# Kernel optimization log

Hardware: AMD Instinct MI355X
Metric: run time of the kernel (lower is better)

Reference implementation:

```python
import jax, jax.numpy as jnp
import numpy as np
from jax import lax

BN_EPS = 1e-5

def ste_sign(x):
    # forward: sign(x) (sign(0)=0, matching torch.sign); backward handled in fwdbwd variant
    return jnp.sign(x)

def setup_inputs() -> dict:
    key = jax.random.key(0)
    k1, k2, k3 = jax.random.split(key, 3)
    x = jax.random.normal(k1, (32, 256, 56, 56), dtype=jnp.float32)
    gamma = jnp.ones((256,), dtype=jnp.float32)
    beta = jnp.zeros((256,), dtype=jnp.float32)
    weight = jax.random.normal(k2, (256, 256, 3, 3), dtype=jnp.float32) * 0.05
    bias = jax.random.normal(k3, (256,), dtype=jnp.float32) * 0.05
    return {"x": x, "gamma": gamma, "beta": beta, "weight": weight, "bias": bias}

def reference(x, gamma, beta, weight, bias):
    # shuffle_groups == 1 -> no channel shuffle
    # BatchNorm2d in training mode: batch statistics over (N, H, W)
    mean = jnp.mean(x, axis=(0, 2, 3), keepdims=True)          # (1,C,1,1)
    var = jnp.var(x, axis=(0, 2, 3), keepdims=True)
    xn = (x - mean) * lax.rsqrt(var + BN_EPS)
    xn = xn * gamma[None, :, None, None] + beta[None, :, None, None]
    # Binary activation: sign
    xb = ste_sign(xn)
    # Binarized-weight conv (weights -> sign(W)), stride 1, padding 1
    wb = ste_sign(weight)
    y = lax.conv_general_dilated(
        xb, wb,
        window_strides=(1, 1),
        padding=[(1, 1), (1, 1)],
        dimension_numbers=("NCHW", "OIHW", "NCHW"),
    )
    y = y + bias[None, :, None, None]
    return jax.nn.relu(y)
```

## Files before the change

### kernel.cpp

```cpp
#include <hip/hip_runtime.h>
#include <stdint.h>


#define CH   256
#define HH   56
#define WW   56
#define HWSZ (HH*WW)
#define NBATCH 32
#define NHW  (NBATCH*HWSZ)


__global__ __launch_bounds__(256) void bn_stats(const float* __restrict__ x,
                                                float* __restrict__ stats,
                                                unsigned* __restrict__ flags) {
    int c = blockIdx.x;
    const float4* xp = (const float4*)x;
    double s = 0.0, s2 = 0.0;
    for (int idx = threadIdx.x; idx < NBATCH * 784; idx += 256) {
        int n = idx / 784, i = idx - n * 784;
        float4 v = xp[(size_t)(n * CH + c) * 784 + i];
        s  += (double)v.x + (double)v.y + (double)v.z + (double)v.w;
        s2 += (double)v.x * v.x + (double)v.y * v.y
            + (double)v.z * v.z + (double)v.w * v.w;
    }
    __shared__ double ls[256], ls2[256];
    ls[threadIdx.x] = s; ls2[threadIdx.x] = s2;
    __syncthreads();
    for (int o = 128; o > 0; o >>= 1) {
        if (threadIdx.x < o) {
            ls[threadIdx.x]  += ls[threadIdx.x + o];
            ls2[threadIdx.x] += ls2[threadIdx.x + o];
        }
        __syncthreads();
    }
    if (threadIdx.x == 0) {
        double mean = ls[0] / (double)NHW;
        double var  = ls2[0] / (double)NHW - mean * mean;
        double istd = 1.0 / sqrt(var + 1e-5);
        stats[2 * c]     = (float)mean;
        stats[2 * c + 1] = (float)istd;
        if (c == 0) *flags = 0u;
    }
}

__global__ __launch_bounds__(256) void binarize(const float* __restrict__ x,
                                                const float* __restrict__ gamma,
                                                const float* __restrict__ beta,
                                                const float* __restrict__ stats,
                                                unsigned long long* __restrict__ Apack,
                                                unsigned long long* __restrict__ Amask,
                                                unsigned* __restrict__ flags) {
    int b = blockIdx.x;
    int n = b / HH, h = b - n * HH;
    __shared__ float lds[CH][WW + 1];
    for (int i = threadIdx.x; i < CH * WW; i += 256) {
        int ci = i / WW, w = i - ci * WW;
        lds[ci][w] = x[(size_t)(n * CH + ci) * HWSZ + h * WW + w];
    }
    __syncthreads();
    int ci = threadIdx.x;
    float m = stats[2 * ci], istd = stats[2 * ci + 1];
    float g = gamma[ci], bb = beta[ci];
    int wv = threadIdx.x >> 6, lane = threadIdx.x & 63;
    bool anyz = false;
    size_t pixbase = (size_t)(n * HH + h) * WW * 4;
    for (int w = 0; w < WW; ++w) {
        float xn = (lds[ci][w] - m) * istd;
        xn = xn * g + bb;
        unsigned long long sb = __ballot(xn > 0.0f);
        unsigned long long mb = __ballot(xn != 0.0f);
        anyz |= (xn == 0.0f);
        if (lane == 0) {
            Apack[pixbase + w * 4 + wv] = sb;
            Amask[pixbase + w * 4 + wv] = mb;
        }
    }
    if (__any(anyz)) { if (lane == 0) atomicOr(flags, 1u); }
}

__global__ __launch_bounds__(128) void packw(const float* __restrict__ wt,
                                             unsigned* __restrict__ Wsign,
                                             unsigned* __restrict__ Wmask,
                                             unsigned* __restrict__ flags) {
    int co = blockIdx.x, t = threadIdx.x;
    if (t >= 72) return;
    int tap = t >> 3, word = t & 7;
    unsigned sb = 0u, mb = 0u;
    for (int j = 0; j < 32; ++j) {
        float v = wt[((size_t)co * CH + (word * 32 + j)) * 9 + tap];
        sb |= (v > 0.0f ? 1u : 0u) << j;
        mb |= (v != 0.0f ? 1u : 0u) << j;
    }
    Wsign[(co * 9 + tap) * 8 + word] = sb;
    Wmask[(co * 9 + tap) * 8 + word] = mb;
    if (mb != 0xffffffffu) atomicOr(flags, 2u);
}

__global__ __launch_bounds__(256) void bconv(const uint32_t* __restrict__ Apack,
                                             const uint32_t* __restrict__ Amask,
                                             const uint32_t* __restrict__ Wsign,
                                             const uint32_t* __restrict__ Wmask,
                                             const float* __restrict__ bias,
                                             const unsigned* __restrict__ flags,
                                             float* __restrict__ out) {
    int b = blockIdx.x;
    int n = b / 28, tb = b - n * 28;
    int h0 = tb * 2;
    int co = threadIdx.x;

    __shared__ __align__(16) uint32_t As[4][WW][8];
    __shared__ __align__(16) uint32_t Am[4][WW][8];

    bool slow = (*flags != 0u);

    int rlo = max(h0 - 1, 0), rhi = min(h0 + 2, HH - 1);
    int nw = (rhi - rlo + 1) * WW * 8;
    {
        const uint4* s4 = (const uint4*)(Apack + (size_t)(n * HH + rlo) * WW * 8);
        uint4* d4 = (uint4*)&As[rlo - (h0 - 1)][0][0];
        for (int i = threadIdx.x; i < nw / 4; i += 256) d4[i] = s4[i];
        if (slow) {
            const uint4* s4m = (const uint4*)(Amask + (size_t)(n * HH + rlo) * WW * 8);
            uint4* d4m = (uint4*)&Am[rlo - (h0 - 1)][0][0];
            for (int i = threadIdx.x; i < nw / 4; i += 256) d4m[i] = s4m[i];
        }
    }

    uint32_t wreg[72];
    #pragma unroll
    for (int i = 0; i < 72; ++i) wreg[i] = Wsign[co * 72 + i];
    float bi = bias[co];
    __syncthreads();

    if (!slow) {
        for (int r = 0; r < 2; ++r) {
            int h = h0 + r;
            size_t obase = (size_t)(n * CH + co) * HWSZ + (size_t)h * WW;
            for (int c = 0; c < WW; ++c) {
                int acc = 0, kcnt = 0;
                #pragma unroll
                for (int kh = 0; kh < 3; ++kh) {
                    int hh = h - 1 + kh;
                    if (hh < 0 || hh >= HH) continue;
                    int lr = r + kh;
                    #pragma unroll
                    for (int kw = 0; kw < 3; ++kw) {
                        int wwc = c - 1 + kw;
                        if (wwc < 0 || wwc >= WW) continue;
                        const uint32_t* ap = &As[lr][wwc][0];
                        #pragma unroll
                        for (int k = 0; k < 8; ++k)
                            acc += __popc(ap[k] ^ wreg[(kh * 3 + kw) * 8 + k]);
                        kcnt += 256;
                    }
                }
                float o = (float)(kcnt - 2 * acc) + bi;
                out[obase + c] = o > 0.0f ? o : 0.0f;
            }
        }
    } else {
        for (int r = 0; r < 2; ++r) {
            int h = h0 + r;
            size_t obase = (size_t)(n * CH + co) * HWSZ + (size_t)h * WW;
            for (int c = 0; c < WW; ++c) {
                int acc = 0, kcnt = 0;
                #pragma unroll
                for (int kh = 0; kh < 3; ++kh) {
                    int hh = h - 1 + kh;
                    if (hh < 0 || hh >= HH) continue;
                    int lr = r + kh;
                    #pragma unroll
                    for (int kw = 0; kw < 3; ++kw) {
                        int wwc = c - 1 + kw;
                        if (wwc < 0 || wwc >= WW) continue;
                        const uint32_t* ap = &As[lr][wwc][0];
                        const uint32_t* am = &Am[lr][wwc][0];
                        const uint32_t* wm = Wmask + (co * 9 + kh * 3 + kw) * 8;
                        #pragma unroll
                        for (int k = 0; k < 8; ++k) {
                            uint32_t M = am[k] & wm[k];
                            kcnt += __popc(M);
                            acc  += __popc((ap[k] ^ wreg[(kh * 3 + kw) * 8 + k]) & M);
                        }
                    }
                }
                float o = (float)(kcnt - 2 * acc) + bi;
                out[obase + c] = o > 0.0f ? o : 0.0f;
            }
        }
    }
}

extern "C" void kernel_launch(void* const* d_in, const int* in_sizes, int n_in,
                              void* d_out, int out_size, void* d_ws, size_t ws_size,
                              hipStream_t stream) {
    const float* x     = (const float*)d_in[0];
    const float* gamma = (const float*)d_in[1];
    const float* beta  = (const float*)d_in[2];
    const float* wt    = (const float*)d_in[3];
    const float* bias  = (const float*)d_in[4];
    float* out = (float*)d_out;

    char* ws = (char*)d_ws;
    float*    stats = (float*)(ws);
    unsigned* flags = (unsigned*)(ws + 2048);
    uint32_t* Wsign = (uint32_t*)(ws + 4096);
    uint32_t* Wmask = (uint32_t*)(ws + 77824);
    uint32_t* Apack = (uint32_t*)(ws + 151552);
    uint32_t* Amask = (uint32_t*)(ws + 3362816);

    hipLaunchKernelGGL(bn_stats, dim3(256), dim3(256), 0, stream, x, stats, flags);
    hipLaunchKernelGGL(binarize, dim3(NBATCH * HH), dim3(256), 0, stream,
                       x, gamma, beta, stats,
                       (unsigned long long*)Apack, (unsigned long long*)Amask, flags);
    hipLaunchKernelGGL(packw, dim3(256), dim3(128), 0, stream, wt, Wsign, Wmask, flags);
    hipLaunchKernelGGL(bconv, dim3(NBATCH * 28), dim3(256), 0, stream,
                       Apack, Amask, Wsign, Wmask, bias, flags, out);
}
```

Measured before the change: 481.2 us.

## Split BN stats, stage binarize writes, and restructure fast binary conv per-pixel

Batch-norm statistics now run as a two-stage reduction over (channel, batch) blocks with wave shuffles, which spreads the work across many more workgroups. Binarize loads with float4 and writes its packed words through LDS as coalesced uint4 stores. The fast convolution path is rewritten so each thread holds one pixel's zero-padded 3x3 window in registers and loops over output channels, reading broadcast weights. A precomputed per-border correction term replaces the per-tap boundary branches. The slow masked path moves to a separate kernel that exits early when not needed, which adds an extra launch, and the 72-word register window may limit occupancy.

```diff
diff --git a/kernel.cpp b/kernel.cpp
--- a/kernel.cpp
+++ b/kernel.cpp
@@ -10,37 +10,46 @@
 #define NHW  (NBATCH*HWSZ)
 
 
-__global__ __launch_bounds__(256) void bn_stats(const float* __restrict__ x,
-                                                float* __restrict__ stats,
-                                                unsigned* __restrict__ flags) {
-    int c = blockIdx.x;
-    const float4* xp = (const float4*)x;
+__global__ __launch_bounds__(256) void bn_partial(const float* __restrict__ x,
+                                                  double* __restrict__ psum,
+                                                  double* __restrict__ psum2) {
+    int b = blockIdx.x;
+    int c = b >> 5, n = b & 31;
+    const float4* x4 = (const float4*)x + (size_t)(n * CH + c) * 784;
     double s = 0.0, s2 = 0.0;
-    for (int idx = threadIdx.x; idx < NBATCH * 784; idx += 256) {
-        int n = idx / 784, i = idx - n * 784;
-        float4 v = xp[(size_t)(n * CH + c) * 784 + i];
+    for (int i = threadIdx.x; i < 784; i += 256) {
+        float4 v = x4[i];
         s  += (double)v.x + (double)v.y + (double)v.z + (double)v.w;
         s2 += (double)v.x * v.x + (double)v.y * v.y
             + (double)v.z * v.z + (double)v.w * v.w;
     }
-    __shared__ double ls[256], ls2[256];
-    ls[threadIdx.x] = s; ls2[threadIdx.x] = s2;
-    __syncthreads();
-    for (int o = 128; o > 0; o >>= 1) {
-        if (threadIdx.x < o) {
-            ls[threadIdx.x]  += ls[threadIdx.x + o];
-            ls2[threadIdx.x] += ls2[threadIdx.x + o];
-        }
-        __syncthreads();
-    }
+    for (int o = 32; o > 0; o >>= 1) {
+        s  += __shfl_down(s, o);
+        s2 += __shfl_down(s2, o);
+    }
+    __shared__ double ls[4], ls2[4];
+    int wv = threadIdx.x >> 6, lane = threadIdx.x & 63;
+    if (lane == 0) { ls[wv] = s; ls2[wv] = s2; }
+    __syncthreads();
     if (threadIdx.x == 0) {
-        double mean = ls[0] / (double)NHW;
-        double var  = ls2[0] / (double)NHW - mean * mean;
-        double istd = 1.0 / sqrt(var + 1e-5);
-        stats[2 * c]     = (float)mean;
-        stats[2 * c + 1] = (float)istd;
-        if (c == 0) *flags = 0u;
-    }
+        psum[b]  = ls[0] + ls[1] + ls[2] + ls[3];
+        psum2[b] = ls2[0] + ls2[1] + ls2[2] + ls2[3];
+    }
+}
+
+__global__ __launch_bounds__(256) void bn_final(const double* __restrict__ psum,
+                                                const double* __restrict__ psum2,
+                                                float* __restrict__ stats,
+                                                unsigned* __restrict__ flags) {
+    int c = threadIdx.x;
+    double s = 0.0, s2 = 0.0;
+    for (int n = 0; n < 32; ++n) { s += psum[c * 32 + n]; s2 += psum2[c * 32 + n]; }
+    double mean = s / (double)NHW;
+    double var  = s2 / (double)NHW - mean * mean;
+    double istd = 1.0 / sqrt(var + 1e-5);
+    stats[2 * c]     = (float)mean;
+    stats[2 * c + 1] = (float)istd;
+    if (c == 0) *flags = 0u;
 }
 
 __global__ __launch_bounds__(256) void binarize(const float* __restrict__ x,
@@ -52,141 +61,207 @@
                                                 unsigned* __restrict__ flags) {
     int b = blockIdx.x;
     int n = b / HH, h = b - n * HH;
-    __shared__ float lds[CH][WW + 1];
-    for (int i = threadIdx.x; i < CH * WW; i += 256) {
-        int ci = i / WW, w = i - ci * WW;
-        lds[ci][w] = x[(size_t)(n * CH + ci) * HWSZ + h * WW + w];
-    }
-    __syncthreads();
-    int ci = threadIdx.x;
+    __shared__ float lds[CH][57];
+    __shared__ __align__(16) unsigned long long pb[WW][4], mb[WW][4];
+    const float4* x4 = (const float4*)x;
+    for (int i = threadIdx.x; i < CH * 14; i += 256) {
+        int ci = i / 14, jj = i - ci * 14;
+        float4 v = x4[(size_t)(n * CH + ci) * 784 + h * 14 + jj];
+        lds[ci][jj * 4 + 0] = v.x;
+        lds[ci][jj * 4 + 1] = v.y;
+        lds[ci][jj * 4 + 2] = v.z;
+        lds[ci][jj * 4 + 3] = v.w;
+    }
+    __syncthreads();
+    int ci = threadIdx.x, wv = ci >> 6, lane = ci & 63;
     float m = stats[2 * ci], istd = stats[2 * ci + 1];
-    float g = gamma[ci], bb = beta[ci];
-    int wv = threadIdx.x >> 6, lane = threadIdx.x & 63;
+    float g = gamma[ci], be = beta[ci];
     bool anyz = false;
-    size_t pixbase = (size_t)(n * HH + h) * WW * 4;
+    #pragma unroll 4
     for (int w = 0; w < WW; ++w) {
-        float xn = (lds[ci][w] - m) * istd;
-        xn = xn * g + bb;
-        unsigned long long sb = __ballot(xn > 0.0f);
-        unsigned long long mb = __ballot(xn != 0.0f);
+        float t  = (lds[ci][w] - m) * istd;
+        float xn = t * g + be;
+        unsigned long long sb  = __ballot(xn > 0.0f);
+        unsigned long long mbv = __ballot(xn != 0.0f);
         anyz |= (xn == 0.0f);
-        if (lane == 0) {
-            Apack[pixbase + w * 4 + wv] = sb;
-            Amask[pixbase + w * 4 + wv] = mb;
-        }
-    }
-    if (__any(anyz)) { if (lane == 0) atomicOr(flags, 1u); }
+        if (lane == 0) { pb[w][wv] = sb; mb[w][wv] = mbv; }
+    }
+    if (__any(anyz) && lane == 0) atomicOr(flags, 1u);
+    __syncthreads();
+    const uint4* ps = (const uint4*)&pb[0][0];
+    const uint4* pm = (const uint4*)&mb[0][0];
+    uint4* go = (uint4*)(Apack + (size_t)b * 224);
+    uint4* gm = (uint4*)(Amask + (size_t)b * 224);
+    for (int i = threadIdx.x; i < 112; i += 256) go[i] = ps[i];
+    for (int i = threadIdx.x; i < 112; i += 256) gm[i] = pm[i];
 }
 
 __global__ __launch_bounds__(128) void packw(const float* __restrict__ wt,
-                                             unsigned* __restrict__ Wsign,
-                                             unsigned* __restrict__ Wmask,
+                                             uint32_t* __restrict__ Wsign,
+                                             uint32_t* __restrict__ Wmask,
+                                             int* __restrict__ corr,
                                              unsigned* __restrict__ flags) {
     int co = blockIdx.x, t = threadIdx.x;
-    if (t >= 72) return;
-    int tap = t >> 3, word = t & 7;
-    unsigned sb = 0u, mb = 0u;
-    for (int j = 0; j < 32; ++j) {
-        float v = wt[((size_t)co * CH + (word * 32 + j)) * 9 + tap];
-        sb |= (v > 0.0f ? 1u : 0u) << j;
-        mb |= (v != 0.0f ? 1u : 0u) << j;
-    }
-    Wsign[(co * 9 + tap) * 8 + word] = sb;
-    Wmask[(co * 9 + tap) * 8 + word] = mb;
-    if (mb != 0xffffffffu) atomicOr(flags, 2u);
-}
-
-__global__ __launch_bounds__(256) void bconv(const uint32_t* __restrict__ Apack,
-                                             const uint32_t* __restrict__ Amask,
-                                             const uint32_t* __restrict__ Wsign,
-                                             const uint32_t* __restrict__ Wmask,
-                                             const float* __restrict__ bias,
-                                             const unsigned* __restrict__ flags,
-                                             float* __restrict__ out) {
+    __shared__ int wpc[72];
+    if (t < 72) {
+        int tap = t >> 3, word = t & 7;
+        unsigned sb = 0u, mbv = 0u;
+        for (int j = 0; j < 32; ++j) {
+            float v = wt[((size_t)co * CH + (word * 32 + j)) * 9 + tap];
+            sb  |= (v > 0.0f ? 1u : 0u) << j;
+            mbv |= (v != 0.0f ? 1u : 0u) << j;
+        }
+        Wsign[co * 72 + tap * 8 + word] = sb;
+        Wmask[co * 72 + tap * 8 + word] = mbv;
+        wpc[tap * 8 + word] = __popc(sb);
+        if (mbv != 0xffffffffu) atomicOr(flags, 2u);
+    }
+    __syncthreads();
+    if (t < 9) {
+        int cfgH = t / 3, cfgW = t % 3;
+        int s = 0;
+        for (int tap = 0; tap < 9; ++tap) {
+            int kh = tap / 3, kw = tap % 3;
+            bool inv = (cfgH == 1 && kh == 0) || (cfgH == 2 && kh == 2) ||
+                       (cfgW == 1 && kw == 0) || (cfgW == 2 && kw == 2);
+            if (inv) {
+                int p = 0;
+                for (int k = 0; k < 8; ++k) p += wpc[tap * 8 + k];
+                s += 256 - 2 * p;
+            }
+        }
+        corr[co * 9 + t] = s;
+    }
+}
+
+__global__ __launch_bounds__(128) void bconv_fast(const uint32_t* __restrict__ Apack,
+                                                  const uint32_t* __restrict__ Wsign,
+                                                  const int* __restrict__ corr,
+                                                  const float* __restrict__ bias,
+                                                  const unsigned* __restrict__ flags,
+                                                  float* __restrict__ out) {
+    if (*flags != 0u) return;
+    __shared__ __align__(16) uint32_t As[6][58][8];
+    __shared__ int corr_lds[2304];
+    __shared__ float bias_lds[CH];
+    int bb = blockIdx.x;
+    int cs = bb & 1;
+    int b  = bb >> 1;
+    int n  = b / 25, pt = b % 25;
+    int pix0 = pt * 128;
+    int pix  = pix0 + threadIdx.x;
+    bool valid = pix < HWSZ;
+    int pixc = valid ? pix : HWSZ - 1;
+    int h = pixc / WW, w = pixc - h * WW;
+    int h0 = pix0 / WW;
+
+    const uint4* Ap4 = (const uint4*)Apack + (size_t)n * (HWSZ * 2);
+    for (int i = threadIdx.x; i < 696; i += 128) {
+        int r = i / 116, j = i - r * 116;
+        int col = j >> 1, half = j & 1;
+        int gr = h0 - 1 + r;
+        uint4 val = make_uint4(0u, 0u, 0u, 0u);
+        if (gr >= 0 && gr < HH && col >= 1 && col <= WW)
+            val = Ap4[(gr * WW + (col - 1)) * 2 + half];
+        *(uint4*)&As[r][col][half * 4] = val;
+    }
+    for (int i = threadIdx.x; i < 576; i += 128)
+        ((uint4*)corr_lds)[i] = ((const uint4*)corr)[i];
+    for (int i = threadIdx.x; i < CH; i += 128)
+        bias_lds[i] = bias[i];
+    __syncthreads();
+
+    uint32_t win[72];
+    int lh = h - h0;
+    #pragma unroll
+    for (int kh = 0; kh < 3; ++kh) {
+        #pragma unroll
+        for (int kw = 0; kw < 3; ++kw) {
+            const uint4* p = (const uint4*)&As[lh + kh][w + kw][0];
+            uint4 lo = p[0], hi = p[1];
+            int t = (kh * 3 + kw) * 8;
+            win[t + 0] = lo.x; win[t + 1] = lo.y; win[t + 2] = lo.z; win[t + 3] = lo.w;
+            win[t + 4] = hi.x; win[t + 5] = hi.y; win[t + 6] = hi.z; win[t + 7] = hi.w;
+        }
+    }
+    int cfg = ((h == 0) ? 1 : (h == HH - 1) ? 2 : 0) * 3
+            + ((w == 0) ? 1 : (w == WW - 1) ? 2 : 0);
+    size_t obase = (size_t)n * (CH * HWSZ) + pix;
+    int co0 = cs * 128;
+    #pragma unroll 1
+    for (int coi = 0; coi < 128; ++coi) {
+        int co = co0 + coi;
+        const uint32_t* wp = Wsign + co * 72;
+        int a0 = 0, a1 = 0, a2 = 0, a3 = 0;
+        #pragma unroll
+        for (int i = 0; i < 72; i += 4) {
+            a0 += __popc(win[i + 0] ^ wp[i + 0]);
+            a1 += __popc(win[i + 1] ^ wp[i + 1]);
+            a2 += __popc(win[i + 2] ^ wp[i + 2]);
+            a3 += __popc(win[i + 3] ^ wp[i + 3]);
+        }
+        int ival = 2304 - 2 * ((a0 + a1) + (a2 + a3)) - corr_lds[co * 9 + cfg];
+        float o = (float)ival + bias_lds[co];
+        o = o > 0.0f ? o : 0.0f;
+        if (valid) out[obase + (size_t)co * HWSZ] = o;
+    }
+}
+
+__global__ __launch_bounds__(256) void bconv_slow(const uint32_t* __restrict__ Apack,
+                                                  const uint32_t* __restrict__ Amask,
+                                                  const uint32_t* __restrict__ Wsign,
+                                                  const uint32_t* __restrict__ Wmask,
+                                                  const float* __restrict__ bias,
+                                                  const unsigned* __restrict__ flags,
+                                                  float* __restrict__ out) {
+    if (*flags == 0u) return;
     int b = blockIdx.x;
     int n = b / 28, tb = b - n * 28;
     int h0 = tb * 2;
     int co = threadIdx.x;
-
     __shared__ __align__(16) uint32_t As[4][WW][8];
     __shared__ __align__(16) uint32_t Am[4][WW][8];
-
-    bool slow = (*flags != 0u);
-
     int rlo = max(h0 - 1, 0), rhi = min(h0 + 2, HH - 1);
     int nw = (rhi - rlo + 1) * WW * 8;
     {
-        const uint4* s4 = (const uint4*)(Apack + (size_t)(n * HH + rlo) * WW * 8);
-        uint4* d4 = (uint4*)&As[rlo - (h0 - 1)][0][0];
-        for (int i = threadIdx.x; i < nw / 4; i += 256) d4[i] = s4[i];
-        if (slow) {
-            const uint4* s4m = (const uint4*)(Amask + (size_t)(n * HH + rlo) * WW * 8);
-            uint4* d4m = (uint4*)&Am[rlo - (h0 - 1)][0][0];
-            for (int i = threadIdx.x; i < nw / 4; i += 256) d4m[i] = s4m[i];
-        }
-    }
-
+        const uint4* s4  = (const uint4*)(Apack + (size_t)(n * HH + rlo) * WW * 8);
+        const uint4* s4m = (const uint4*)(Amask + (size_t)(n * HH + rlo) * WW * 8);
+        uint4* d4  = (uint4*)&As[rlo - (h0 - 1)][0][0];
+        uint4* d4m = (uint4*)&Am[rlo - (h0 - 1)][0][0];
+        for (int i = threadIdx.x; i < nw / 4; i += 256) { d4[i] = s4[i]; d4m[i] = s4m[i]; }
+    }
     uint32_t wreg[72];
     #pragma unroll
     for (int i = 0; i < 72; ++i) wreg[i] = Wsign[co * 72 + i];
     float bi = bias[co];
     __syncthreads();
-
-    if (!slow) {
-        for (int r = 0; r < 2; ++r) {
-            int h = h0 + r;
-            size_t obase = (size_t)(n * CH + co) * HWSZ + (size_t)h * WW;
-            for (int c = 0; c < WW; ++c) {
-                int acc = 0, kcnt = 0;
+    for (int r = 0; r < 2; ++r) {
+        int h = h0 + r;
+        size_t obase = (size_t)(n * CH + co) * HWSZ + (size_t)h * WW;
+        for (int c = 0; c < WW; ++c) {
+            int acc = 0, kcnt = 0;
+            #pragma unroll
+            for (int kh = 0; kh < 3; ++kh) {
+                int hh = h - 1 + kh;
+                if (hh < 0 || hh >= HH) continue;
+                int lr = r + kh;
                 #pragma unroll
-                for (int kh = 0; kh < 3; ++kh) {
-                    int hh = h - 1 + kh;
-                    if (hh < 0 || hh >= HH) continue;
-                    int lr = r + kh;
+                for (int kw = 0; kw < 3; ++kw) {
+                    int wwc = c - 1 + kw;
+                    if (wwc < 0 || wwc >= WW) continue;
+                    const uint32_t* ap = &As[lr][wwc][0];
+                    const uint32_t* am = &Am[lr][wwc][0];
+                    const uint32_t* wm = Wmask + (co * 9 + kh * 3 + kw) * 8;
                     #pragma unroll
-                    for (int kw = 0; kw < 3; ++kw) {
-                        int wwc = c - 1 + kw;
-                        if (wwc < 0 || wwc >= WW) continue;
-                        const uint32_t* ap = &As[lr][wwc][0];
-                        #pragma unroll
-                        for (int k = 0; k < 8; ++k)
-                            acc += __popc(ap[k] ^ wreg[(kh * 3 + kw) * 8 + k]);
-                        kcnt += 256;
+                    for (int k = 0; k < 8; ++k) {
+                        uint32_t M = am[k] & wm[k];
+                        kcnt += __popc(M);
+                        acc  += __popc((ap[k] ^ wreg[(kh * 3 + kw) * 8 + k]) & M);
                     }
                 }
-                float o = (float)(kcnt - 2 * acc) + bi;
-                out[obase + c] = o > 0.0f ? o : 0.0f;
             }
-        }
-    } else {
-        for (int r = 0; r < 2; ++r) {
-            int h = h0 + r;
-            size_t obase = (size_t)(n * CH + co) * HWSZ + (size_t)h * WW;
-            for (int c = 0; c < WW; ++c) {
-                int acc = 0, kcnt = 0;
-                #pragma unroll
-                for (int kh = 0; kh < 3; ++kh) {
-                    int hh = h - 1 + kh;
-                    if (hh < 0 || hh >= HH) continue;
-                    int lr = r + kh;
-                    #pragma unroll
-                    for (int kw = 0; kw < 3; ++kw) {
-                        int wwc = c - 1 + kw;
-                        if (wwc < 0 || wwc >= WW) continue;
-                        const uint32_t* ap = &As[lr][wwc][0];
-                        const uint32_t* am = &Am[lr][wwc][0];
-                        const uint32_t* wm = Wmask + (co * 9 + kh * 3 + kw) * 8;
-                        #pragma unroll
-                        for (int k = 0; k < 8; ++k) {
-                            uint32_t M = am[k] & wm[k];
-                            kcnt += __popc(M);
-                            acc  += __popc((ap[k] ^ wreg[(kh * 3 + kw) * 8 + k]) & M);
-                        }
-                    }
-                }
-                float o = (float)(kcnt - 2 * acc) + bi;
-                out[obase + c] = o > 0.0f ? o : 0.0f;
-            }
+            float o = (float)(kcnt - 2 * acc) + bi;
+            out[obase + c] = o > 0.0f ? o : 0.0f;
         }
     }
 }
@@ -204,16 +279,22 @@
     char* ws = (char*)d_ws;
     float*    stats = (float*)(ws);
     unsigned* flags = (unsigned*)(ws + 2048);
-    uint32_t* Wsign = (uint32_t*)(ws + 4096);
-    uint32_t* Wmask = (uint32_t*)(ws + 77824);
-    uint32_t* Apack = (uint32_t*)(ws + 151552);
-    uint32_t* Amask = (uint32_t*)(ws + 3362816);
-
-    hipLaunchKernelGGL(bn_stats, dim3(256), dim3(256), 0, stream, x, stats, flags);
+    int*      corr  = (int*)(ws + 4096);
+    uint32_t* Wsign = (uint32_t*)(ws + 16384);
+    uint32_t* Wmask = (uint32_t*)(ws + 90112);
+    uint32_t* Apack = (uint32_t*)(ws + 163840);
+    uint32_t* Amask = (uint32_t*)(ws + 3375104);
+    double*   psum  = (double*)(ws + 163840);
+    double*   psum2 = (double*)(ws + 163840 + 65536);
+
+    hipLaunchKernelGGL(bn_partial, dim3(8192), dim3(256), 0, stream, x, psum, psum2);
+    hipLaunchKernelGGL(bn_final, dim3(1), dim3(256), 0, stream, psum, psum2, stats, flags);
     hipLaunchKernelGGL(binarize, dim3(NBATCH * HH), dim3(256), 0, stream,
                        x, gamma, beta, stats,
                        (unsigned long long*)Apack, (unsigned long long*)Amask, flags);
-    hipLaunchKernelGGL(packw, dim3(256), dim3(128), 0, stream, wt, Wsign, Wmask, flags);
-    hipLaunchKernelGGL(bconv, dim3(NBATCH * 28), dim3(256), 0, stream,
+    hipLaunchKernelGGL(packw, dim3(256), dim3(128), 0, stream, wt, Wsign, Wmask, corr, flags);
+    hipLaunchKernelGGL(bconv_fast, dim3(1600), dim3(128), 0, stream,
+                       Apack, Wsign, corr, bias, flags, out);
+    hipLaunchKernelGGL(bconv_slow, dim3(NBATCH * 28), dim3(256), 0, stream,
                        Apack, Amask, Wsign, Wmask, bias, flags, out);
 }
```

After: 392.2 us. 18.5% less time.
